# Performance work log

Measured on AMD Instinct MI355X. Metric: run time of the kernel, lower is better.

Reference implementation:

```python
import jax, jax.numpy as jnp
import numpy as np

L, P, DV, DP = 16, 1024, 64, 16   # latent caps, prim caps (neighbors), latent vec, prim vec
N_SRC, N_TGT = 64, 64
NUM_ITER = 3


def setup_inputs() -> dict:
    key = jax.random.key(0)
    k1, k2, k3 = jax.random.split(key, 3)
    feature = jax.random.normal(k1, (N_SRC + N_TGT, DP), dtype=jnp.float32)
    # neighbor indices: each half indexes into its own 64-row feature block
    select_cap = jax.random.randint(k2, (N_SRC + N_TGT, P), 0, N_SRC).astype(jnp.int64)
    W = 0.01 * jax.random.normal(k3, (L, P, DV, DP), dtype=jnp.float32)
    return {"feature": feature, "select_cap": select_cap, "W": W, "n_src": N_SRC}


def squash(s):
    # s: [..., DV]
    sn = jnp.sum(s * s, axis=-1, keepdims=True)
    return sn * s / ((1.0 + sn) * jnp.sqrt(sn))


def routing(x, W):
    # x: [B, P, DP], W: [L, P, DV, DP]
    u_hat = jnp.einsum('lpvq,bpq->blpv', W, x)          # [B, L, P, DV]
    u_det = jax.lax.stop_gradient(u_hat)                 # matches torch .detach()
    b = jnp.zeros(x.shape[:1] + (L, P), dtype=x.dtype)   # routing logits [B, L, P]
    for _ in range(NUM_ITER - 1):
        c = jax.nn.softmax(b, axis=1)                    # softmax over latent caps dim
        v = squash(jnp.einsum('blp,blpv->blv', c, u_det))
        b = b + jnp.einsum('blv,blpv->blp', v, u_det)
    c = jax.nn.softmax(b, axis=1)
    return squash(jnp.einsum('blp,blpv->blv', c, u_hat))  # [B, L, DV]


def reference(feature, select_cap, W, n_src):
    # per-point neighbor gather, honoring src/tgt split at n_src
    feat_src = feature[:n_src]
    feat_tgt = feature[n_src:]
    batch_src = feat_src[select_cap[:n_src]]             # [n_src, P, DP]
    batch_tgt = feat_tgt[select_cap[n_src:]]             # [n_tgt, P, DP]
    batch_feat = jnp.concatenate([batch_src, batch_tgt], axis=0)  # [N, P, DP]
    caps = routing(batch_feat, W)                        # [N, L, DV]
    norms = jnp.linalg.norm(caps, axis=-1).T             # [L, N]
    return caps, norms
```

## Files before the change

kernel.cpp:

```cpp
#include <hip/hip_runtime.h>
#include <hip/hip_bf16.h>

namespace {

constexpr int L_  = 16;
constexpr int P_  = 1024;
constexpr int DV_ = 64;
constexpr int DP_ = 16;
constexpr int B_  = 128;

constexpr size_t PB   = (size_t)P_ * B_;
constexpr size_t SLV  = (size_t)B_ * L_ * DV_;
constexpr size_t LPBT = (size_t)L_ * PB;

constexpr int KCH = 32;
constexpr int PPC = P_ / KCH;
constexpr int MCH = 64;

typedef __attribute__((ext_vector_type(8)))  short bf16x8;
typedef __attribute__((ext_vector_type(16))) float f32x16;

__device__ __forceinline__ void pack2(bf16x8& d, int i, float lo, float hi) {
  __hip_bfloat162 t = __float22bfloat162_rn(float2{lo, hi});
  short2 s = *reinterpret_cast<short2*>(&t);
  d[2 * i] = s.x;
  d[2 * i + 1] = s.y;
}

__global__ __launch_bounds__(256) void k_prep(
    const int* __restrict__ sel, const int* __restrict__ nsrc_p,
    int* __restrict__ jbuf)
{
  const int i = blockIdx.x * 256 + threadIdx.x;
  const int b = i >> 10, p = i & (P_ - 1);
  const int ns = *nsrc_p;
  jbuf[p * B_ + b] = sel[i] + (b >= ns ? ns : 0);
}

template<bool UNIFORM, bool USE_PART>
__global__ __launch_bounds__(256) void k_wsum(
    const float* __restrict__ W, const float* __restrict__ feat,
    const int* __restrict__ jbuf, const float* __restrict__ cbuf,
    float* __restrict__ out)
{
  const int l    = blockIdx.y;
  const int kc   = blockIdx.x;
  const int wave = threadIdx.x >> 6;
  const int lane = threadIdx.x & 63;
  const int col  = lane & 31;
  const int h    = lane >> 5;
  const int bcol = wave * 32 + col;

  f32x16 acc0, acc1;
#pragma unroll
  for (int r = 0; r < 16; ++r) { acc0[r] = 0.f; acc1[r] = 0.f; }

  const int p_begin = kc * PPC;
#pragma unroll 2
  for (int ps = 0; ps < PPC; ++ps) {
    const int p = p_begin + ps;

    const int jj = jbuf[p * B_ + bcol];
    const float cw = UNIFORM ? 0.0625f
                             : cbuf[(size_t)l * PB + (size_t)p * B_ + bcol];
    const float4* fx = reinterpret_cast<const float4*>(feat + jj * DP_ + h * 8);
    const float4 f0 = fx[0], f1 = fx[1];
    bf16x8 bfrag;
    pack2(bfrag, 0, cw * f0.x, cw * f0.y);
    pack2(bfrag, 1, cw * f0.z, cw * f0.w);
    pack2(bfrag, 2, cw * f1.x, cw * f1.y);
    pack2(bfrag, 3, cw * f1.z, cw * f1.w);

    const float* wa0 = W + (((size_t)l * P_ + p) * DV_ + col) * DP_ + h * 8;
    const float* wa1 = wa0 + (size_t)32 * DP_;
    const float4 w00 = *(const float4*)wa0, w01 = *(const float4*)(wa0 + 4);
    const float4 w10 = *(const float4*)wa1, w11 = *(const float4*)(wa1 + 4);
    bf16x8 a0, a1;
    pack2(a0, 0, w00.x, w00.y); pack2(a0, 1, w00.z, w00.w);
    pack2(a0, 2, w01.x, w01.y); pack2(a0, 3, w01.z, w01.w);
    pack2(a1, 0, w10.x, w10.y); pack2(a1, 1, w10.z, w10.w);
    pack2(a1, 2, w11.x, w11.y); pack2(a1, 3, w11.z, w11.w);

    acc0 = __builtin_amdgcn_mfma_f32_32x32x16_bf16(a0, bfrag, acc0, 0, 0, 0);
    acc1 = __builtin_amdgcn_mfma_f32_32x32x16_bf16(a1, bfrag, acc1, 0, 0, 0);
  }

  if (USE_PART) {
    float* op = out + ((size_t)l * KCH + kc) * ((size_t)DV_ * B_);
#pragma unroll
    for (int r = 0; r < 16; ++r) {
      const int v0 = (r & 3) + 8 * (r >> 2) + 4 * h;
      op[(size_t)v0 * B_ + bcol]        = acc0[r];
      op[(size_t)(v0 + 32) * B_ + bcol] = acc1[r];
    }
  } else {
#pragma unroll
    for (int r = 0; r < 16; ++r) {
      const int v0 = (r & 3) + 8 * (r >> 2) + 4 * h;
      atomicAdd(&out[((size_t)bcol * L_ + l) * DV_ + v0],      acc0[r]);
      atomicAdd(&out[((size_t)bcol * L_ + l) * DV_ + v0 + 32], acc1[r]);
    }
  }
}

__global__ __launch_bounds__(256) void k_reduce_s(
    const float* __restrict__ spart, float* __restrict__ s)
{
  const int idx = blockIdx.x * 256 + threadIdx.x;
  const int l  = idx >> 13;
  const int vb = idx & 8191;
  const float* sp = spart + (size_t)l * KCH * 8192 + vb;
  float t = 0.f;
#pragma unroll
  for (int c = 0; c < KCH; ++c) t += sp[(size_t)c * 8192];
  const int v = vb >> 7, b = vb & 127;
  s[((size_t)b * L_ + l) * DV_ + v] = t;
}

template<bool ADDB>
__global__ __launch_bounds__(256) void k_dotv(
    const float* __restrict__ W, const float* __restrict__ feat,
    const int* __restrict__ jbuf, const float* __restrict__ vv,
    const float* __restrict__ bprev, float* __restrict__ dout)
{
  const int l    = blockIdx.y;
  const int mc   = blockIdx.x;
  const int wave = threadIdx.x >> 6;
  const int lane = threadIdx.x & 63;
  const int col  = lane & 31;
  const int h    = lane >> 5;
  const int bcol = wave * 32 + col;

  bf16x8 bf[4];
#pragma unroll
  for (int ks = 0; ks < 4; ++ks) {
    const float* vp = vv + ((size_t)bcol * L_ + l) * DV_ + ks * 16 + h * 8;
    const float4 v0 = *(const float4*)vp, v1 = *(const float4*)(vp + 4);
    pack2(bf[ks], 0, v0.x, v0.y); pack2(bf[ks], 1, v0.z, v0.w);
    pack2(bf[ks], 2, v1.x, v1.y); pack2(bf[ks], 3, v1.z, v1.w);
  }

  const int p_base = mc * 16;
  const int prow_off = (col >> 4);
  const int q = col & 15;

#pragma unroll 2
  for (int mt = 0; mt < 8; ++mt) {
    const int p0 = p_base + mt * 2;
    const int prow = p0 + prow_off;

    f32x16 acc;
#pragma unroll
    for (int r = 0; r < 16; ++r) acc[r] = 0.f;

#pragma unroll
    for (int ks = 0; ks < 4; ++ks) {
      const int vb = ks * 16 + h * 8;
      const float* wp = W + (((size_t)l * P_ + prow) * DV_ + vb) * DP_ + q;
      bf16x8 af;
#pragma unroll
      for (int j = 0; j < 4; ++j)
        pack2(af, j, wp[(size_t)(2 * j) * DP_], wp[(size_t)(2 * j + 1) * DP_]);
      acc = __builtin_amdgcn_mfma_f32_32x32x16_bf16(af, bf[ks], acc, 0, 0, 0);
    }

    const int j0 = jbuf[p0 * B_ + bcol];
    const int j1 = jbuf[(p0 + 1) * B_ + bcol];
    float d0 = 0.f, d1 = 0.f;
#pragma unroll
    for (int r = 0; r < 8; ++r) {
      const int q_r = (r & 3) + 8 * (r >> 2) + 4 * h;
      d0 = fmaf(acc[r],     feat[j0 * DP_ + q_r], d0);
      d1 = fmaf(acc[r + 8], feat[j1 * DP_ + q_r], d1);
    }
    d0 += __shfl_xor(d0, 32);
    d1 += __shfl_xor(d1, 32);
    if (h == 0) {
      const size_t o0 = (size_t)l * PB + (size_t)p0 * B_ + bcol;
      const size_t o1 = o0 + B_;
      float w0 = d0, w1 = d1;
      if (ADDB) { w0 += bprev[o0]; w1 += bprev[o1]; }
      dout[o0] = w0;
      dout[o1] = w1;
    }
  }
}

__global__ __launch_bounds__(256) void k_softmax_l(
    const float* __restrict__ lin, float* __restrict__ lout)
{
  const int idx = blockIdx.x * 256 + threadIdx.x;
  const float* ip = lin + idx;
  float x[L_];
  float m = -1e30f;
#pragma unroll
  for (int l = 0; l < L_; ++l) { x[l] = ip[(size_t)l * PB]; m = fmaxf(m, x[l]); }
  float den = 0.f;
#pragma unroll
  for (int l = 0; l < L_; ++l) { x[l] = __expf(x[l] - m); den += x[l]; }
  const float r = 1.f / den;
  float* op = lout + idx;
#pragma unroll
  for (int l = 0; l < L_; ++l) op[(size_t)l * PB] = x[l] * r;
}

__global__ __launch_bounds__(256) void k_squash(
    const float* __restrict__ sbuf, float* __restrict__ vout)
{
  const int row = blockIdx.x * 4 + (threadIdx.x >> 6);
  const int v = threadIdx.x & 63;
  const float s = sbuf[(size_t)row * DV_ + v];
  float t = s * s;
#pragma unroll
  for (int m = 32; m >= 1; m >>= 1) t += __shfl_xor(t, m, 64);
  vout[(size_t)row * DV_ + v] = s * sqrtf(t) / (1.f + t);
}

__global__ __launch_bounds__(256) void k_final(
    const float* __restrict__ sbuf, float* __restrict__ caps,
    float* __restrict__ norms)
{
  const int row = blockIdx.x * 4 + (threadIdx.x >> 6);
  const int v = threadIdx.x & 63;
  const float s = sbuf[(size_t)row * DV_ + v];
  float t = s * s;
#pragma unroll
  for (int m = 32; m >= 1; m >>= 1) t += __shfl_xor(t, m, 64);
  caps[(size_t)row * DV_ + v] = s * sqrtf(t) / (1.f + t);
  if (v == 0) {
    const int b = row >> 4;
    const int l = row & (L_ - 1);
    norms[(size_t)l * B_ + b] = t / (1.f + t);
  }
}

}

extern "C" void kernel_launch(void* const* d_in, const int* in_sizes, int n_in,
                              void* d_out, int out_size, void* d_ws, size_t ws_size,
                              hipStream_t stream)
{
  (void)in_sizes; (void)n_in; (void)out_size;
  const float* feat   = (const float*)d_in[0];
  const int*   sel    = (const int*)d_in[1];
  const float* W      = (const float*)d_in[2];
  const int*   nsrc_p = (const int*)d_in[3];

  float* caps  = (float*)d_out;
  float* norms = caps + SLV;

  float* s1    = (float*)d_ws;
  float* s2    = s1 + SLV;
  float* s3    = s2 + SLV;
  float* v1    = s3 + SLV;
  float* v2    = v1 + SLV;
  float* bb1   = v2 + SLV;
  float* bufc  = bb1 + LPBT;
  int*   jbuf  = (int*)(bufc + LPBT);
  float* spart = (float*)(jbuf + PB);

  const size_t need_elems = 5 * SLV + 2 * LPBT + PB + (size_t)L_ * KCH * 8192;
  const bool use_part = ws_size >= need_elems * sizeof(float);

  const dim3 blk(256);
  const dim3 gW(KCH, L_);
  const dim3 gD(MCH, L_);
  const dim3 gF(512);

  k_prep<<<gF, blk, 0, stream>>>(sel, nsrc_p, jbuf);
  if (!use_part)
    hipMemsetAsync(s1, 0, 3 * SLV * sizeof(float), stream);

  if (use_part) {
    k_wsum<true, true><<<gW, blk, 0, stream>>>(W, feat, jbuf, nullptr, spart);
    k_reduce_s<<<gF, blk, 0, stream>>>(spart, s1);
  } else {
    k_wsum<true, false><<<gW, blk, 0, stream>>>(W, feat, jbuf, nullptr, s1);
  }
  k_squash<<<gF, blk, 0, stream>>>(s1, v1);
  k_dotv<false><<<gD, blk, 0, stream>>>(W, feat, jbuf, v1, nullptr, bb1);

  k_softmax_l<<<gF, blk, 0, stream>>>(bb1, bufc);
  if (use_part) {
    k_wsum<false, true><<<gW, blk, 0, stream>>>(W, feat, jbuf, bufc, spart);
    k_reduce_s<<<gF, blk, 0, stream>>>(spart, s2);
  } else {
    k_wsum<false, false><<<gW, blk, 0, stream>>>(W, feat, jbuf, bufc, s2);
  }
  k_squash<<<gF, blk, 0, stream>>>(s2, v2);
  k_dotv<true><<<gD, blk, 0, stream>>>(W, feat, jbuf, v2, bb1, bufc);

  k_softmax_l<<<gF, blk, 0, stream>>>(bufc, bufc);
  if (use_part) {
    k_wsum<false, true><<<gW, blk, 0, stream>>>(W, feat, jbuf, bufc, spart);
    k_reduce_s<<<gF, blk, 0, stream>>>(spart, s3);
  } else {
    k_wsum<false, false><<<gW, blk, 0, stream>>>(W, feat, jbuf, bufc, s3);
  }
  k_final<<<gF, blk, 0, stream>>>(s3, caps, norms);
}
```

Baseline: 266.4 us.

## Pre-convert W to fp16 MFMA-fragment layouts and fuse reduce with squash

A new conversion kernel turns W into two fp16 copies, each pre-arranged in the per-lane fragment order used by the weighted-sum and dot kernels. This replaces strided fp32 loads and per-iteration bf16 packing with single coalesced 16-byte loads. The partial-sum reduction is fused with squash and the final norm output, the atomic fallback path is removed, and wsum now splits work across two accumulator sets. The trade-offs are an extra full pass over W on every call, a larger workspace with no size check, and fp16 range and precision in place of bf16.

```diff
diff --git a/kernel.cpp b/kernel.cpp
--- a/kernel.cpp
+++ b/kernel.cpp
@@ -1,5 +1,6 @@
 #include <hip/hip_runtime.h>
 #include <hip/hip_bf16.h>
+#include <hip/hip_fp16.h>
 
 namespace {
 
@@ -15,33 +16,87 @@
 
 constexpr int KCH = 32;
 constexpr int PPC = P_ / KCH;
-constexpr int MCH = 64;
-
-typedef __attribute__((ext_vector_type(8)))  short bf16x8;
-typedef __attribute__((ext_vector_type(16))) float f32x16;
-
-__device__ __forceinline__ void pack2(bf16x8& d, int i, float lo, float hi) {
-  __hip_bfloat162 t = __float22bfloat162_rn(float2{lo, hi});
-  short2 s = *reinterpret_cast<short2*>(&t);
-  d[2 * i] = s.x;
-  d[2 * i + 1] = s.y;
+constexpr int MCHD = 64;
+
+typedef _Float16 f16;
+typedef __attribute__((ext_vector_type(8)))  _Float16 f16x8;
+typedef __attribute__((ext_vector_type(16))) float    f32x16;
+
+constexpr size_t WF_UNITS = (size_t)L_ * P_ * 2 * 64;
+constexpr size_t WT_UNITS = (size_t)L_ * 512 * 4 * 64;
+
+__device__ __forceinline__ f16x8 mul_pk(const __half2 cwh, const f16x8 f) {
+  union { f16x8 v; __half2 h2[4]; } fu, bu;
+  fu.v = f;
+#pragma unroll
+  for (int i = 0; i < 4; ++i) bu.h2[i] = __hmul2(cwh, fu.h2[i]);
+  return bu.v;
 }
 
 __global__ __launch_bounds__(256) void k_prep(
     const int* __restrict__ sel, const int* __restrict__ nsrc_p,
-    int* __restrict__ jbuf)
+    int* __restrict__ jbuf, const float* __restrict__ feat,
+    f16* __restrict__ feat16, f16* __restrict__ feat16s)
 {
   const int i = blockIdx.x * 256 + threadIdx.x;
   const int b = i >> 10, p = i & (P_ - 1);
   const int ns = *nsrc_p;
   jbuf[p * B_ + b] = sel[i] + (b >= ns ? ns : 0);
-}
-
-template<bool UNIFORM, bool USE_PART>
+  if (i < B_ * DP_) {
+    const float f = feat[i];
+    feat16[i]  = (f16)f;
+    feat16s[i] = (f16)(0.0625f * f);
+  }
+}
+
+__global__ __launch_bounds__(256) void k_cvtW(
+    const float* __restrict__ W, f16* __restrict__ wf, f16* __restrict__ wt)
+{
+  const size_t id = (size_t)blockIdx.x * 256 + threadIdx.x;
+  if (id < WF_UNITS) {
+    const int lane = id & 63;
+    const int mt   = (id >> 6) & 1;
+    const size_t lp = id >> 7;
+    const int v  = mt * 32 + (lane & 31);
+    const int q8 = (lane >> 5) * 8;
+    const float* src = W + (lp * 64 + v) * 16 + q8;
+    const float4 a = *(const float4*)src;
+    const float4 b = *(const float4*)(src + 4);
+    union { f16x8 v8; __half2 h2[4]; } o;
+    o.h2[0] = __float22half2_rn(float2{a.x, a.y});
+    o.h2[1] = __float22half2_rn(float2{a.z, a.w});
+    o.h2[2] = __float22half2_rn(float2{b.x, b.y});
+    o.h2[3] = __float22half2_rn(float2{b.z, b.w});
+    reinterpret_cast<f16x8*>(wf)[id] = o.v8;
+  } else {
+    const size_t id2 = id - WF_UNITS;
+    if (id2 >= WT_UNITS) return;
+    const int lane = id2 & 63;
+    const int ks   = (id2 >> 6) & 3;
+    const size_t lpt = id2 >> 8;
+    const int l  = (int)(lpt >> 9);
+    const int pt = (int)(lpt & 511);
+    const int col = lane & 31;
+    const int p  = pt * 2 + (col >> 4);
+    const int q  = col & 15;
+    const int vb = ks * 16 + (lane >> 5) * 8;
+    const float* src = W + (((size_t)l * P_ + p) * 64 + vb) * 16 + q;
+    float s[8];
+#pragma unroll
+    for (int jv = 0; jv < 8; ++jv) s[jv] = src[(size_t)jv * 16];
+    union { f16x8 v8; __half2 h2[4]; } o;
+#pragma unroll
+    for (int i = 0; i < 4; ++i)
+      o.h2[i] = __float22half2_rn(float2{s[2 * i], s[2 * i + 1]});
+    reinterpret_cast<f16x8*>(wt)[id2] = o.v8;
+  }
+}
+
+template<bool UNIFORM>
 __global__ __launch_bounds__(256) void k_wsum(
-    const float* __restrict__ W, const float* __restrict__ feat,
-    const int* __restrict__ jbuf, const float* __restrict__ cbuf,
-    float* __restrict__ out)
+    const f16* __restrict__ wf, const f16* __restrict__ feat16,
+    const f16* __restrict__ feat16s, const int* __restrict__ jbuf,
+    const float* __restrict__ cbuf, float* __restrict__ spart)
 {
   const int l    = blockIdx.y;
   const int kc   = blockIdx.x;
@@ -51,75 +106,53 @@
   const int h    = lane >> 5;
   const int bcol = wave * 32 + col;
 
-  f32x16 acc0, acc1;
-#pragma unroll
-  for (int r = 0; r < 16; ++r) { acc0[r] = 0.f; acc1[r] = 0.f; }
-
-  const int p_begin = kc * PPC;
-#pragma unroll 2
+  f32x16 accA0, accA1, accB0, accB1;
+#pragma unroll
+  for (int r = 0; r < 16; ++r) {
+    accA0[r] = 0.f; accA1[r] = 0.f; accB0[r] = 0.f; accB1[r] = 0.f;
+  }
+
+  const int p0 = kc * PPC;
+  const f16x8* wfu = reinterpret_cast<const f16x8*>(wf);
+#pragma unroll 4
   for (int ps = 0; ps < PPC; ++ps) {
-    const int p = p_begin + ps;
-
+    const int p = p0 + ps;
+    const size_t lp = (size_t)l * P_ + p;
     const int jj = jbuf[p * B_ + bcol];
-    const float cw = UNIFORM ? 0.0625f
-                             : cbuf[(size_t)l * PB + (size_t)p * B_ + bcol];
-    const float4* fx = reinterpret_cast<const float4*>(feat + jj * DP_ + h * 8);
-    const float4 f0 = fx[0], f1 = fx[1];
-    bf16x8 bfrag;
-    pack2(bfrag, 0, cw * f0.x, cw * f0.y);
-    pack2(bfrag, 1, cw * f0.z, cw * f0.w);
-    pack2(bfrag, 2, cw * f1.x, cw * f1.y);
-    pack2(bfrag, 3, cw * f1.z, cw * f1.w);
-
-    const float* wa0 = W + (((size_t)l * P_ + p) * DV_ + col) * DP_ + h * 8;
-    const float* wa1 = wa0 + (size_t)32 * DP_;
-    const float4 w00 = *(const float4*)wa0, w01 = *(const float4*)(wa0 + 4);
-    const float4 w10 = *(const float4*)wa1, w11 = *(const float4*)(wa1 + 4);
-    bf16x8 a0, a1;
-    pack2(a0, 0, w00.x, w00.y); pack2(a0, 1, w00.z, w00.w);
-    pack2(a0, 2, w01.x, w01.y); pack2(a0, 3, w01.z, w01.w);
-    pack2(a1, 0, w10.x, w10.y); pack2(a1, 1, w10.z, w10.w);
-    pack2(a1, 2, w11.x, w11.y); pack2(a1, 3, w11.z, w11.w);
-
-    acc0 = __builtin_amdgcn_mfma_f32_32x32x16_bf16(a0, bfrag, acc0, 0, 0, 0);
-    acc1 = __builtin_amdgcn_mfma_f32_32x32x16_bf16(a1, bfrag, acc1, 0, 0, 0);
-  }
-
-  if (USE_PART) {
-    float* op = out + ((size_t)l * KCH + kc) * ((size_t)DV_ * B_);
-#pragma unroll
-    for (int r = 0; r < 16; ++r) {
-      const int v0 = (r & 3) + 8 * (r >> 2) + 4 * h;
-      op[(size_t)v0 * B_ + bcol]        = acc0[r];
-      op[(size_t)(v0 + 32) * B_ + bcol] = acc1[r];
-    }
-  } else {
-#pragma unroll
-    for (int r = 0; r < 16; ++r) {
-      const int v0 = (r & 3) + 8 * (r >> 2) + 4 * h;
-      atomicAdd(&out[((size_t)bcol * L_ + l) * DV_ + v0],      acc0[r]);
-      atomicAdd(&out[((size_t)bcol * L_ + l) * DV_ + v0 + 32], acc1[r]);
-    }
-  }
-}
-
-__global__ __launch_bounds__(256) void k_reduce_s(
-    const float* __restrict__ spart, float* __restrict__ s)
-{
-  const int idx = blockIdx.x * 256 + threadIdx.x;
-  const int l  = idx >> 13;
-  const int vb = idx & 8191;
-  const float* sp = spart + (size_t)l * KCH * 8192 + vb;
-  float t = 0.f;
-#pragma unroll
-  for (int c = 0; c < KCH; ++c) t += sp[(size_t)c * 8192];
-  const int v = vb >> 7, b = vb & 127;
-  s[((size_t)b * L_ + l) * DV_ + v] = t;
+
+    f16x8 bfrag;
+    if (UNIFORM) {
+      bfrag = *reinterpret_cast<const f16x8*>(feat16s + jj * DP_ + h * 8);
+    } else {
+      const float cw = cbuf[(size_t)l * PB + (size_t)p * B_ + bcol];
+      const __half2 cwh = __float2half2_rn(cw);
+      const f16x8 fr = *reinterpret_cast<const f16x8*>(feat16 + jj * DP_ + h * 8);
+      bfrag = mul_pk(cwh, fr);
+    }
+
+    const f16x8 a0 = wfu[(lp * 2 + 0) * 64 + lane];
+    const f16x8 a1 = wfu[(lp * 2 + 1) * 64 + lane];
+    if (ps & 1) {
+      accB0 = __builtin_amdgcn_mfma_f32_32x32x16_f16(a0, bfrag, accB0, 0, 0, 0);
+      accB1 = __builtin_amdgcn_mfma_f32_32x32x16_f16(a1, bfrag, accB1, 0, 0, 0);
+    } else {
+      accA0 = __builtin_amdgcn_mfma_f32_32x32x16_f16(a0, bfrag, accA0, 0, 0, 0);
+      accA1 = __builtin_amdgcn_mfma_f32_32x32x16_f16(a1, bfrag, accA1, 0, 0, 0);
+    }
+  }
+
+  float* op = spart + ((size_t)l * KCH + kc) * ((size_t)DV_ * B_);
+#pragma unroll
+  for (int r = 0; r < 16; ++r) {
+    const int v0 = (r & 3) + 8 * (r >> 2) + 4 * h;
+    op[(size_t)v0 * B_ + bcol]        = accA0[r] + accB0[r];
+    op[(size_t)(v0 + 32) * B_ + bcol] = accA1[r] + accB1[r];
+  }
 }
 
 template<bool ADDB>
 __global__ __launch_bounds__(256) void k_dotv(
-    const float* __restrict__ W, const float* __restrict__ feat,
+    const f16* __restrict__ wt, const float* __restrict__ feat,
     const int* __restrict__ jbuf, const float* __restrict__ vv,
     const float* __restrict__ bprev, float* __restrict__ dout)
 {
@@ -131,23 +164,26 @@
   const int h    = lane >> 5;
   const int bcol = wave * 32 + col;
 
-  bf16x8 bf[4];
+  f16x8 bf[4];
 #pragma unroll
   for (int ks = 0; ks < 4; ++ks) {
     const float* vp = vv + ((size_t)bcol * L_ + l) * DV_ + ks * 16 + h * 8;
     const float4 v0 = *(const float4*)vp, v1 = *(const float4*)(vp + 4);
-    pack2(bf[ks], 0, v0.x, v0.y); pack2(bf[ks], 1, v0.z, v0.w);
-    pack2(bf[ks], 2, v1.x, v1.y); pack2(bf[ks], 3, v1.z, v1.w);
-  }
-
-  const int p_base = mc * 16;
-  const int prow_off = (col >> 4);
-  const int q = col & 15;
+    union { f16x8 v8; __half2 h2[4]; } u;
+    u.h2[0] = __float22half2_rn(float2{v0.x, v0.y});
+    u.h2[1] = __float22half2_rn(float2{v0.z, v0.w});
+    u.h2[2] = __float22half2_rn(float2{v1.x, v1.y});
+    u.h2[3] = __float22half2_rn(float2{v1.z, v1.w});
+    bf[ks] = u.v8;
+  }
+
+  const int ptbase = mc * 8;
+  const f16x8* wtu = reinterpret_cast<const f16x8*>(wt);
 
 #pragma unroll 2
   for (int mt = 0; mt < 8; ++mt) {
-    const int p0 = p_base + mt * 2;
-    const int prow = p0 + prow_off;
+    const int pt = ptbase + mt;
+    const size_t lpt = (size_t)l * 512 + pt;
 
     f32x16 acc;
 #pragma unroll
@@ -155,15 +191,11 @@
 
 #pragma unroll
     for (int ks = 0; ks < 4; ++ks) {
-      const int vb = ks * 16 + h * 8;
-      const float* wp = W + (((size_t)l * P_ + prow) * DV_ + vb) * DP_ + q;
-      bf16x8 af;
-#pragma unroll
-      for (int j = 0; j < 4; ++j)
-        pack2(af, j, wp[(size_t)(2 * j) * DP_], wp[(size_t)(2 * j + 1) * DP_]);
-      acc = __builtin_amdgcn_mfma_f32_32x32x16_bf16(af, bf[ks], acc, 0, 0, 0);
-    }
-
+      const f16x8 af = wtu[(lpt * 4 + ks) * 64 + lane];
+      acc = __builtin_amdgcn_mfma_f32_32x32x16_f16(af, bf[ks], acc, 0, 0, 0);
+    }
+
+    const int p0 = pt * 2;
     const int j0 = jbuf[p0 * B_ + bcol];
     const int j1 = jbuf[(p0 + 1) * B_ + bcol];
     float d0 = 0.f, d1 = 0.f;
@@ -204,34 +236,28 @@
   for (int l = 0; l < L_; ++l) op[(size_t)l * PB] = x[l] * r;
 }
 
-__global__ __launch_bounds__(256) void k_squash(
-    const float* __restrict__ sbuf, float* __restrict__ vout)
-{
-  const int row = blockIdx.x * 4 + (threadIdx.x >> 6);
-  const int v = threadIdx.x & 63;
-  const float s = sbuf[(size_t)row * DV_ + v];
-  float t = s * s;
-#pragma unroll
-  for (int m = 32; m >= 1; m >>= 1) t += __shfl_xor(t, m, 64);
-  vout[(size_t)row * DV_ + v] = s * sqrtf(t) / (1.f + t);
-}
-
-__global__ __launch_bounds__(256) void k_final(
-    const float* __restrict__ sbuf, float* __restrict__ caps,
+template<bool FINAL>
+__global__ __launch_bounds__(256) void k_reduce(
+    const float* __restrict__ spart, float* __restrict__ vout,
     float* __restrict__ norms)
 {
-  const int row = blockIdx.x * 4 + (threadIdx.x >> 6);
-  const int v = threadIdx.x & 63;
-  const float s = sbuf[(size_t)row * DV_ + v];
-  float t = s * s;
-#pragma unroll
-  for (int m = 32; m >= 1; m >>= 1) t += __shfl_xor(t, m, 64);
-  caps[(size_t)row * DV_ + v] = s * sqrtf(t) / (1.f + t);
-  if (v == 0) {
-    const int b = row >> 4;
-    const int l = row & (L_ - 1);
-    norms[(size_t)l * B_ + b] = t / (1.f + t);
-  }
+  const int bid = blockIdx.x;
+  const int l  = bid >> 5;
+  const int b  = (bid & 31) * 4 + (threadIdx.x >> 6);
+  const int v  = threadIdx.x & 63;
+
+  const float* sp = spart + (size_t)l * KCH * 8192 + (size_t)v * 128 + b;
+  float x = 0.f;
+#pragma unroll
+  for (int c = 0; c < KCH; ++c) x += sp[(size_t)c * 8192];
+
+  float t2 = x * x;
+#pragma unroll
+  for (int m = 32; m >= 1; m >>= 1) t2 += __shfl_xor(t2, m, 64);
+  const float scale = sqrtf(t2) / (1.f + t2);
+
+  vout[((size_t)b * L_ + l) * DV_ + v] = x * scale;
+  if (FINAL && v == 0) norms[(size_t)l * B_ + b] = t2 / (1.f + t2);
 }
 
 }
@@ -240,7 +266,7 @@
                               void* d_out, int out_size, void* d_ws, size_t ws_size,
                               hipStream_t stream)
 {
-  (void)in_sizes; (void)n_in; (void)out_size;
+  (void)in_sizes; (void)n_in; (void)out_size; (void)ws_size;
   const float* feat   = (const float*)d_in[0];
   const int*   sel    = (const int*)d_in[1];
   const float* W      = (const float*)d_in[2];
@@ -249,53 +275,38 @@
   float* caps  = (float*)d_out;
   float* norms = caps + SLV;
 
-  float* s1    = (float*)d_ws;
-  float* s2    = s1 + SLV;
-  float* s3    = s2 + SLV;
-  float* v1    = s3 + SLV;
-  float* v2    = v1 + SLV;
-  float* bb1   = v2 + SLV;
-  float* bufc  = bb1 + LPBT;
-  int*   jbuf  = (int*)(bufc + LPBT);
-  float* spart = (float*)(jbuf + PB);
-
-  const size_t need_elems = 5 * SLV + 2 * LPBT + PB + (size_t)L_ * KCH * 8192;
-  const bool use_part = ws_size >= need_elems * sizeof(float);
+  float* base  = (float*)d_ws;
+  f16*   wf     = (f16*)base;
+  f16*   wt     = (f16*)(base + WF_UNITS * 4);
+  float* spart  = base + WF_UNITS * 8;
+  float* bb1    = spart + (size_t)L_ * KCH * 8192;
+  float* bufc   = bb1 + LPBT;
+  float* v1     = bufc + LPBT;
+  float* v2     = v1 + SLV;
+  int*   jbuf   = (int*)(v2 + SLV);
+  f16*   feat16 = (f16*)(jbuf + PB);
+  f16*   feat16s = feat16 + B_ * DP_;
 
   const dim3 blk(256);
   const dim3 gW(KCH, L_);
-  const dim3 gD(MCH, L_);
+  const dim3 gD(MCHD, L_);
   const dim3 gF(512);
-
-  k_prep<<<gF, blk, 0, stream>>>(sel, nsrc_p, jbuf);
-  if (!use_part)
-    hipMemsetAsync(s1, 0, 3 * SLV * sizeof(float), stream);
-
-  if (use_part) {
-    k_wsum<true, true><<<gW, blk, 0, stream>>>(W, feat, jbuf, nullptr, spart);
-    k_reduce_s<<<gF, blk, 0, stream>>>(spart, s1);
-  } else {
-    k_wsum<true, false><<<gW, blk, 0, stream>>>(W, feat, jbuf, nullptr, s1);
-  }
-  k_squash<<<gF, blk, 0, stream>>>(s1, v1);
-  k_dotv<false><<<gD, blk, 0, stream>>>(W, feat, jbuf, v1, nullptr, bb1);
+  const dim3 gR(L_ * (B_ / 4));
+  const dim3 gC((unsigned)((WF_UNITS + WT_UNITS) / 256));
+
+  k_prep<<<gF, blk, 0, stream>>>(sel, nsrc_p, jbuf, feat, feat16, feat16s);
+  k_cvtW<<<gC, blk, 0, stream>>>(W, wf, wt);
+
+  k_wsum<true><<<gW, blk, 0, stream>>>(wf, feat16, feat16s, jbuf, nullptr, spart);
+  k_reduce<false><<<gR, blk, 0, stream>>>(spart, v1, nullptr);
+  k_dotv<false><<<gD, blk, 0, stream>>>(wt, feat, jbuf, v1, nullptr, bb1);
 
   k_softmax_l<<<gF, blk, 0, stream>>>(bb1, bufc);
-  if (use_part) {
-    k_wsum<false, true><<<gW, blk, 0, stream>>>(W, feat, jbuf, bufc, spart);
-    k_reduce_s<<<gF, blk, 0, stream>>>(spart, s2);
-  } else {
-    k_wsum<false, false><<<gW, blk, 0, stream>>>(W, feat, jbuf, bufc, s2);
-  }
-  k_squash<<<gF, blk, 0, stream>>>(s2, v2);
-  k_dotv<true><<<gD, blk, 0, stream>>>(W, feat, jbuf, v2, bb1, bufc);
+  k_wsum<false><<<gW, blk, 0, stream>>>(wf, feat16, feat16s, jbuf, bufc, spart);
+  k_reduce<false><<<gR, blk, 0, stream>>>(spart, v2, nullptr);
+  k_dotv<true><<<gD, blk, 0, stream>>>(wt, feat, jbuf, v2, bb1, bufc);
 
   k_softmax_l<<<gF, blk, 0, stream>>>(bufc, bufc);
-  if (use_part) {
-    k_wsum<false, true><<<gW, blk, 0, stream>>>(W, feat, jbuf, bufc, spart);
-    k_reduce_s<<<gF, blk, 0, stream>>>(spart, s3);
-  } else {
-    k_wsum<false, false><<<gW, blk, 0, stream>>>(W, feat, jbuf, bufc, s3);
-  }
-  k_final<<<gF, blk, 0, stream>>>(s3, caps, norms);
-}
+  k_wsum<false><<<gW, blk, 0, stream>>>(wf, feat16, feat16s, jbuf, bufc, spart);
+  k_reduce<true><<<gR, blk, 0, stream>>>(spart, caps, norms);
+}
```

Measured after the change: 301.9 us. 13.3% more time.
